# Kernel tuning notes

Hardware: AMD Instinct MI355X
Metric: run time of the kernel (lower is better)

## Reference

```python
import jax, jax.numpy as jnp
import numpy as np

E = 128      # n_routed_experts (hardcoded in DS_CONFIG_FOR_NEMOTRON)
I = 1856     # moe_intermediate_size
K = 6        # num_experts_per_tok
H = 512      # config.hidden_size
T = 4096     # flattened tokens (batch*seq)
C = 320      # per-expert capacity; avg load = T*K/E = 192, C=320 makes drops ~impossible


def setup_inputs() -> dict:
    key = jax.random.key(0)
    k1, k2, k3, k4, k5 = jax.random.split(key, 5)
    return {
        "hidden_states": jax.random.normal(k1, (T, H), jnp.float32),
        "top_k_index": jax.random.randint(k2, (T, K), 0, E, jnp.int32),
        "top_k_weights": jax.random.uniform(k3, (T, K), jnp.float32),
        "w_gate_up": jax.random.normal(k4, (E, H, 2 * I), jnp.float32) * 0.02,
        "w_down": jax.random.normal(k5, (E, I, H), jnp.float32) * 0.02,
    }


def reference(hidden_states, top_k_index, top_k_weights, w_gate_up, w_down):
    # Grouped-GEMM formulation of the naive per-expert loop: sort the (token, k)
    # pairs by expert, pack each expert's tokens into a fixed-capacity buffer,
    # run batched gate/up/down GEMMs over all experts at once, then weighted
    # scatter-add back to token order. Same math as the torch loop.
    N = T * K
    e = top_k_index.reshape(N)                      # expert id per pair
    tok = jnp.repeat(jnp.arange(T), K)              # token id per pair
    w = top_k_weights.reshape(N)

    order = jnp.argsort(e)                          # stable sort by expert
    e_s, tok_s, w_s = e[order], tok[order], w[order]

    counts = jax.ops.segment_sum(jnp.ones((N,), jnp.int32), e, num_segments=E)
    starts = jnp.cumsum(counts) - counts            # exclusive prefix sum
    pos = jnp.arange(N) - starts[e_s]               # rank within expert
    valid = pos < C                                 # capacity guard (never trips at this load)
    slot = jnp.where(valid, e_s * C + pos, E * C)   # overflow -> dummy slot

    # Dispatch: [E*C+1, H] buffer of gathered token states (dummy row absorbs overflow)
    buf = jnp.zeros((E * C + 1, H), hidden_states.dtype).at[slot].set(hidden_states[tok_s])
    x = buf[: E * C].reshape(E, C, H)

    gu = jnp.einsum('ech,ehf->ecf', x, w_gate_up)   # [E, C, 2I]
    gate, up = jnp.split(gu, 2, axis=-1)
    inter = jax.nn.silu(gate) * up                  # [E, C, I]
    y = jnp.einsum('eci,eih->ech', inter, w_down).reshape(E * C, H)

    # Combine: gather each pair's expert output, scale by router weight, scatter-add by token
    gather_idx = jnp.where(valid, e_s * C + pos, 0)
    pair_y = y[gather_idx] * jnp.where(valid, w_s, 0.0)[:, None]
    out = jnp.zeros((T, H), hidden_states.dtype).at[tok_s].add(pair_y)
    # use_context_proj=False: context states alias the hidden states
    return (out, out)
```

## Files before the change

### kernel.cpp

```cpp
#include <hip/hip_runtime.h>
#include <hip/hip_bf16.h>
#include <stdint.h>

#define NE 128
#define NI 1856
#define NKK 6
#define NH 512
#define NT 4096
#define CAP 320
#define NPAIR (NT*NKK)
#define LD2I (2*NI)

typedef unsigned short u16;
typedef __attribute__((ext_vector_type(4))) float f32x4;
typedef __attribute__((ext_vector_type(8))) short bf16x8;
typedef __attribute__((ext_vector_type(4))) short s16x4;
typedef const void __attribute__((address_space(1)))* gas1p;
typedef void __attribute__((address_space(3)))* gas3p;

__device__ __forceinline__ short f2bf(float f) {
  union { __hip_bfloat16 h; short s; } c; c.h = __float2bfloat16(f); return c.s;
}
__device__ __forceinline__ float bf2f(short s) {
  union { float f; unsigned u; } v; v.u = ((unsigned)(u16)s) << 16; return v.f;
}

__global__ void k_route(const int* __restrict__ topk, int* __restrict__ counts,
                        int* __restrict__ slot_of_pair, int* __restrict__ pair_of_slot) {
  int n = blockIdx.x * 256 + threadIdx.x;
  if (n >= NPAIR) return;
  int e = topk[n];
  int p = atomicAdd(&counts[e], 1);
  int s = (p < CAP) ? e * CAP + p : -1;
  slot_of_pair[n] = s;
  if (s >= 0) pair_of_slot[s] = n;
}

__global__ void k_gather(const float* __restrict__ hid, const int* __restrict__ counts,
                         const int* __restrict__ pair_of_slot, u16* __restrict__ xbuf) {
  int t = threadIdx.x;
  int row = blockIdx.x * 2 + (t >> 7);
  int c = t & 127;
  int e = row / CAP, p = row % CAP;
  if (p >= counts[e]) return;
  int n = pair_of_slot[row];
  int tok = n / NKK;
  f32x4 v = *(const f32x4*)(hid + (size_t)tok * NH + c * 4);
  s16x4 o;
  o[0] = f2bf(v[0]); o[1] = f2bf(v[1]); o[2] = f2bf(v[2]); o[3] = f2bf(v[3]);
  *(s16x4*)(xbuf + (size_t)row * NH + c * 4) = o;
}

__global__ __launch_bounds__(256, 2) void k_gemm1(
    const u16* __restrict__ xbuf, const float* __restrict__ wgu,
    const int* __restrict__ counts, u16* __restrict__ inter, int e0)
{
  __shared__ __align__(16) char lds[32768];
  int bid = blockIdx.x;
  int mt = bid % 3;
  int nt = (bid / 3) % 29;
  int el = bid / 87;
  int e = e0 + el;
  int cnt = counts[e];
  int row0 = mt * 128;
  if (row0 >= cnt) return;
  int n0 = nt * 64;
  int t = threadIdx.x, w = t >> 6, l = t & 63;
  int wm = w >> 1, wc = w & 1;
  const char* abase = (const char*)(xbuf + (size_t)e * CAP * NH);

  auto stage = [&](int buf, int kt) {
    char* dstb = lds + buf * 16384;
    #pragma unroll
    for (int i = 0; i < 4; ++i) {
      int seg = i * 4 + w;
      int o = seg * 1024 + l * 16;
      int r = o >> 7;
      int inner = o & 127;
      int si = inner ^ ((r & 7) << 4);
      int grow = row0 + r; grow = grow < CAP ? grow : CAP - 1;
      const char* g = abase + (size_t)grow * (NH * 2) + kt * 128 + si;
      __builtin_amdgcn_global_load_lds((gas1p)g, (gas3p)(dstb + seg * 1024), 16, 0, 0);
    }
  };

  f32x4 acc[4][4];
  #pragma unroll
  for (int m = 0; m < 4; ++m)
    #pragma unroll
    for (int b = 0; b < 4; ++b) acc[m][b] = (f32x4){0.f, 0.f, 0.f, 0.f};

  stage(0, 0);
  const float* wbase = wgu + (size_t)e * NH * LD2I + n0 + wc * 32 + (l & 15);

  for (int kt = 0; kt < 8; ++kt) {
    __syncthreads();
    if (kt + 1 < 8) stage((kt + 1) & 1, kt + 1);
    const char* abuf = lds + (kt & 1) * 16384;
    #pragma unroll
    for (int ks = 0; ks < 2; ++ks) {
      int krow = kt * 64 + ks * 32 + ((l >> 4) << 3);
      const float* bp = wbase + (size_t)krow * LD2I;
      float bv[4][8];
      #pragma unroll
      for (int nf = 0; nf < 2; ++nf)
        #pragma unroll
        for (int j = 0; j < 8; ++j) {
          bv[nf][j]     = bp[(size_t)j * LD2I + nf * 16];
          bv[2 + nf][j] = bp[(size_t)j * LD2I + nf * 16 + NI];
        }
      bf16x8 bfrag[4];
      #pragma unroll
      for (int b = 0; b < 4; ++b)
        #pragma unroll
        for (int j = 0; j < 8; ++j) bfrag[b][j] = f2bf(bv[b][j]);
      bf16x8 afrag[4];
      #pragma unroll
      for (int mf = 0; mf < 4; ++mf) {
        int r = wm * 64 + mf * 16 + (l & 15);
        int inner = (ks * 64 + ((l >> 4) << 4)) ^ ((r & 7) << 4);
        afrag[mf] = *(const bf16x8*)(abuf + r * 128 + inner);
      }
      #pragma unroll
      for (int mf = 0; mf < 4; ++mf)
        #pragma unroll
        for (int b = 0; b < 4; ++b)
          acc[mf][b] = __builtin_amdgcn_mfma_f32_16x16x32_bf16(afrag[mf], bfrag[b], acc[mf][b], 0, 0, 0);
    }
  }

  __syncthreads();

  int vmax = cnt < CAP ? cnt : CAP;
  int rmax = vmax - row0; if (rmax > 128) rmax = 128;
  char* rb = lds;
  #pragma unroll
  for (int mf = 0; mf < 4; ++mf)
    #pragma unroll
    for (int nf = 0; nf < 2; ++nf) {
      f32x4 g = acc[mf][nf], u = acc[mf][2 + nf];
      #pragma unroll
      for (int r = 0; r < 4; ++r) {
        float gv = g[r];
        float sv = gv / (1.f + __expf(-gv));
        float val = sv * u[r];
        int rl = wm * 64 + mf * 16 + ((l >> 4) << 2) + r;
        int cl = wc * 32 + nf * 16 + (l & 15);
        *(short*)(rb + rl * 128 + ((cl * 2) ^ ((rl & 7) << 4))) = f2bf(val);
      }
    }
  __syncthreads();
  u16* obase = inter + (size_t)(el * CAP + row0) * NI + n0;
  #pragma unroll
  for (int i = 0; i < 4; ++i) {
    int task = i * 256 + t;
    int r = task >> 3, part = task & 7;
    if (r < rmax) {
      bf16x8 v = *(const bf16x8*)(rb + r * 128 + ((part * 16) ^ ((r & 7) << 4)));
      *(bf16x8*)(obase + (size_t)r * NI + part * 8) = v;
    }
  }
}

__global__ __launch_bounds__(256, 2) void k_gemm2(
    const u16* __restrict__ inter, const float* __restrict__ wdn,
    const int* __restrict__ counts, u16* __restrict__ Y, int e0)
{
  __shared__ __align__(16) char lds[32768];
  int bid = blockIdx.x;
  int mt = bid % 3;
  int nt = (bid / 3) & 7;
  int el = bid / 24;
  int e = e0 + el;
  int cnt = counts[e];
  int row0 = mt * 128;
  if (row0 >= cnt) return;
  int n0 = nt * 64;
  int t = threadIdx.x, w = t >> 6, l = t & 63;
  int wm = w >> 1, wc = w & 1;
  const char* abase = (const char*)(inter + (size_t)el * CAP * NI);

  auto stage = [&](int buf, int kt) {
    char* dstb = lds + buf * 16384;
    #pragma unroll
    for (int i = 0; i < 4; ++i) {
      int seg = i * 4 + w;
      int o = seg * 1024 + l * 16;
      int r = o >> 7;
      int inner = o & 127;
      int si = inner ^ ((r & 7) << 4);
      int grow = row0 + r; grow = grow < CAP ? grow : CAP - 1;
      const char* g = abase + (size_t)grow * (NI * 2) + kt * 128 + si;
      __builtin_amdgcn_global_load_lds((gas1p)g, (gas3p)(dstb + seg * 1024), 16, 0, 0);
    }
  };

  f32x4 acc[4][2];
  #pragma unroll
  for (int m = 0; m < 4; ++m) { acc[m][0] = (f32x4){0.f,0.f,0.f,0.f}; acc[m][1] = (f32x4){0.f,0.f,0.f,0.f}; }

  stage(0, 0);
  const float* wbase = wdn + (size_t)e * NI * NH + n0 + wc * 32 + (l & 15);

  for (int kt = 0; kt < 29; ++kt) {
    __syncthreads();
    if (kt + 1 < 29) stage((kt + 1) & 1, kt + 1);
    const char* abuf = lds + (kt & 1) * 16384;
    #pragma unroll
    for (int ks = 0; ks < 2; ++ks) {
      int krow = kt * 64 + ks * 32 + ((l >> 4) << 3);
      const float* bp = wbase + (size_t)krow * NH;
      float bv[2][8];
      #pragma unroll
      for (int nf = 0; nf < 2; ++nf)
        #pragma unroll
        for (int j = 0; j < 8; ++j) bv[nf][j] = bp[(size_t)j * NH + nf * 16];
      bf16x8 bfrag[2];
      #pragma unroll
      for (int b = 0; b < 2; ++b)
        #pragma unroll
        for (int j = 0; j < 8; ++j) bfrag[b][j] = f2bf(bv[b][j]);
      bf16x8 afrag[4];
      #pragma unroll
      for (int mf = 0; mf < 4; ++mf) {
        int r = wm * 64 + mf * 16 + (l & 15);
        int inner = (ks * 64 + ((l >> 4) << 4)) ^ ((r & 7) << 4);
        afrag[mf] = *(const bf16x8*)(abuf + r * 128 + inner);
      }
      #pragma unroll
      for (int mf = 0; mf < 4; ++mf)
        #pragma unroll
        for (int b = 0; b < 2; ++b)
          acc[mf][b] = __builtin_amdgcn_mfma_f32_16x16x32_bf16(afrag[mf], bfrag[b], acc[mf][b], 0, 0, 0);
    }
  }

  __syncthreads();

  int vmax = cnt < CAP ? cnt : CAP;
  int rmax = vmax - row0; if (rmax > 128) rmax = 128;
  char* rb = lds;
  #pragma unroll
  for (int mf = 0; mf < 4; ++mf)
    #pragma unroll
    for (int nf = 0; nf < 2; ++nf) {
      f32x4 a = acc[mf][nf];
      #pragma unroll
      for (int r = 0; r < 4; ++r) {
        int rl = wm * 64 + mf * 16 + ((l >> 4) << 2) + r;
        int cl = wc * 32 + nf * 16 + (l & 15);
        *(short*)(rb + rl * 128 + ((cl * 2) ^ ((rl & 7) << 4))) = f2bf(a[r]);
      }
    }
  __syncthreads();
  u16* obase = Y + (size_t)(e * CAP + row0) * NH + n0;
  #pragma unroll
  for (int i = 0; i < 4; ++i) {
    int task = i * 256 + t;
    int r = task >> 3, part = task & 7;
    if (r < rmax) {
      bf16x8 v = *(const bf16x8*)(rb + r * 128 + ((part * 16) ^ ((r & 7) << 4)));
      *(bf16x8*)(obase + (size_t)r * NH + part * 8) = v;
    }
  }
}

__global__ void k_combine(const int* __restrict__ slot_of_pair, const float* __restrict__ wts,
                          const u16* __restrict__ Y, float* __restrict__ out)
{
  int t = threadIdx.x;
  int tok = blockIdx.x * 2 + (t >> 7);
  int c = t & 127;
  f32x4 a = (f32x4){0.f, 0.f, 0.f, 0.f};
  #pragma unroll
  for (int k = 0; k < NKK; ++k) {
    int n = tok * NKK + k;
    int s = slot_of_pair[n];
    if (s >= 0) {
      float wv = wts[n];
      s16x4 y = *(const s16x4*)(Y + (size_t)s * NH + c * 4);
      a[0] += wv * bf2f(y[0]);
      a[1] += wv * bf2f(y[1]);
      a[2] += wv * bf2f(y[2]);
      a[3] += wv * bf2f(y[3]);
    }
  }
  *(f32x4*)(out + (size_t)tok * NH + c * 4) = a;
  *(f32x4*)(out + (size_t)(NT + tok) * NH + c * 4) = a;
}

extern "C" void kernel_launch(void* const* d_in, const int* in_sizes, int n_in,
                              void* d_out, int out_size, void* d_ws, size_t ws_size,
                              hipStream_t stream) {
  const float* hid  = (const float*)d_in[0];
  const int*   topk = (const int*)d_in[1];
  const float* wts  = (const float*)d_in[2];
  const float* wgu  = (const float*)d_in[3];
  const float* wdn  = (const float*)d_in[4];

  char* ws = (char*)d_ws;
  size_t off = 0;
  auto alloc = [&](size_t sz) { char* p = ws + off; off = (off + sz + 255) & ~(size_t)255; return p; };
  int* counts        = (int*)alloc(NE * 4);
  int* slot_of_pair  = (int*)alloc((size_t)NPAIR * 4);
  int* pair_of_slot  = (int*)alloc((size_t)NE * CAP * 4);
  u16* xbuf          = (u16*)alloc((size_t)NE * CAP * NH * 2);
  u16* Y             = (u16*)alloc((size_t)NE * CAP * NH * 2);
  size_t remain = ws_size > off ? ws_size - off : 0;
  size_t per_e = (size_t)CAP * NI * 2;
  int chunkE = (int)(remain / per_e);
  if (chunkE > NE) chunkE = NE;
  if (chunkE < 1) chunkE = 1;
  u16* inter = (u16*)(ws + off);

  hipMemsetAsync(counts, 0, NE * 4, stream);
  k_route<<<NPAIR / 256, 256, 0, stream>>>(topk, counts, slot_of_pair, pair_of_slot);
  k_gather<<<NE * CAP / 2, 256, 0, stream>>>(hid, counts, pair_of_slot, xbuf);
  for (int e0 = 0; e0 < NE; e0 += chunkE) {
    int ce = NE - e0 < chunkE ? NE - e0 : chunkE;
    k_gemm1<<<ce * 29 * 3, 256, 0, stream>>>(xbuf, wgu, counts, inter, e0);
    k_gemm2<<<ce * 8 * 3, 256, 0, stream>>>(inter, wdn, counts, Y, e0);
  }
  k_combine<<<NT / 2, 256, 0, stream>>>(slot_of_pair, wts, Y, (float*)d_out);
}
```

Before: 650.9 us.

## Use 256-row M tiles with 512-thread blocks and XCD-aware block remapping

Both grouped GEMMs now use 512-thread blocks covering 256 token rows (two M tiles per expert instead of three), with 64KB LDS double buffers. This halves how often each block re-reads and re-converts the fp32 weight slice, and the weights are the dominant traffic. A block-id remap groups logical neighbours (same expert) onto the same XCD to improve L2 reuse of weights. In exchange, occupancy drops to one block per CU, and experts with fewer rows waste more of the larger tile.

```diff
diff --git a/kernel.cpp b/kernel.cpp
--- a/kernel.cpp
+++ b/kernel.cpp
@@ -23,6 +23,12 @@
 }
 __device__ __forceinline__ float bf2f(short s) {
   union { float f; unsigned u; } v; v.u = ((unsigned)(u16)s) << 16; return v.f;
+}
+
+__device__ __forceinline__ int xcd_logical(int bid, int n) {
+  int q = n >> 3, r = n & 7;
+  int xcd = bid & 7, j = bid >> 3;
+  return xcd * q + (xcd < r ? xcd : r) + j;
 }
 
 __global__ void k_route(const int* __restrict__ topk, int* __restrict__ counts,
@@ -51,18 +57,19 @@
   *(s16x4*)(xbuf + (size_t)row * NH + c * 4) = o;
 }
 
-__global__ __launch_bounds__(256, 2) void k_gemm1(
+__global__ __launch_bounds__(512, 1) void k_gemm1(
     const u16* __restrict__ xbuf, const float* __restrict__ wgu,
-    const int* __restrict__ counts, u16* __restrict__ inter, int e0)
+    const int* __restrict__ counts, u16* __restrict__ inter, int e0, int nblk)
 {
-  __shared__ __align__(16) char lds[32768];
-  int bid = blockIdx.x;
-  int mt = bid % 3;
-  int nt = (bid / 3) % 29;
-  int el = bid / 87;
+  __shared__ __align__(16) char lds[65536];
+  int L = xcd_logical(blockIdx.x, nblk);
+  int el = L / 58;
+  int inner = L % 58;
+  int nt = inner >> 1;
+  int mt = inner & 1;
   int e = e0 + el;
   int cnt = counts[e];
-  int row0 = mt * 128;
+  int row0 = mt * 256;
   if (row0 >= cnt) return;
   int n0 = nt * 64;
   int t = threadIdx.x, w = t >> 6, l = t & 63;
@@ -70,14 +77,14 @@
   const char* abase = (const char*)(xbuf + (size_t)e * CAP * NH);
 
   auto stage = [&](int buf, int kt) {
-    char* dstb = lds + buf * 16384;
+    char* dstb = lds + buf * 32768;
     #pragma unroll
     for (int i = 0; i < 4; ++i) {
-      int seg = i * 4 + w;
+      int seg = i * 8 + w;
       int o = seg * 1024 + l * 16;
       int r = o >> 7;
-      int inner = o & 127;
-      int si = inner ^ ((r & 7) << 4);
+      int inr = o & 127;
+      int si = inr ^ ((r & 7) << 4);
       int grow = row0 + r; grow = grow < CAP ? grow : CAP - 1;
       const char* g = abase + (size_t)grow * (NH * 2) + kt * 128 + si;
       __builtin_amdgcn_global_load_lds((gas1p)g, (gas3p)(dstb + seg * 1024), 16, 0, 0);
@@ -96,7 +103,7 @@
   for (int kt = 0; kt < 8; ++kt) {
     __syncthreads();
     if (kt + 1 < 8) stage((kt + 1) & 1, kt + 1);
-    const char* abuf = lds + (kt & 1) * 16384;
+    const char* abuf = lds + (kt & 1) * 32768;
     #pragma unroll
     for (int ks = 0; ks < 2; ++ks) {
       int krow = kt * 64 + ks * 32 + ((l >> 4) << 3);
@@ -118,8 +125,8 @@
       #pragma unroll
       for (int mf = 0; mf < 4; ++mf) {
         int r = wm * 64 + mf * 16 + (l & 15);
-        int inner = (ks * 64 + ((l >> 4) << 4)) ^ ((r & 7) << 4);
-        afrag[mf] = *(const bf16x8*)(abuf + r * 128 + inner);
+        int inr = (ks * 64 + ((l >> 4) << 4)) ^ ((r & 7) << 4);
+        afrag[mf] = *(const bf16x8*)(abuf + r * 128 + inr);
       }
       #pragma unroll
       for (int mf = 0; mf < 4; ++mf)
@@ -132,7 +139,7 @@
   __syncthreads();
 
   int vmax = cnt < CAP ? cnt : CAP;
-  int rmax = vmax - row0; if (rmax > 128) rmax = 128;
+  int rmax = vmax - row0; if (rmax > 256) rmax = 256;
   char* rb = lds;
   #pragma unroll
   for (int mf = 0; mf < 4; ++mf)
@@ -153,7 +160,7 @@
   u16* obase = inter + (size_t)(el * CAP + row0) * NI + n0;
   #pragma unroll
   for (int i = 0; i < 4; ++i) {
-    int task = i * 256 + t;
+    int task = i * 512 + t;
     int r = task >> 3, part = task & 7;
     if (r < rmax) {
       bf16x8 v = *(const bf16x8*)(rb + r * 128 + ((part * 16) ^ ((r & 7) << 4)));
@@ -162,18 +169,19 @@
   }
 }
 
-__global__ __launch_bounds__(256, 2) void k_gemm2(
+__global__ __launch_bounds__(512, 1) void k_gemm2(
     const u16* __restrict__ inter, const float* __restrict__ wdn,
-    const int* __restrict__ counts, u16* __restrict__ Y, int e0)
+    const int* __restrict__ counts, u16* __restrict__ Y, int e0, int nblk)
 {
-  __shared__ __align__(16) char lds[32768];
-  int bid = blockIdx.x;
-  int mt = bid % 3;
-  int nt = (bid / 3) & 7;
-  int el = bid / 24;
+  __shared__ __align__(16) char lds[65536];
+  int L = xcd_logical(blockIdx.x, nblk);
+  int el = L / 16;
+  int inner = L % 16;
+  int nt = inner >> 1;
+  int mt = inner & 1;
   int e = e0 + el;
   int cnt = counts[e];
-  int row0 = mt * 128;
+  int row0 = mt * 256;
   if (row0 >= cnt) return;
   int n0 = nt * 64;
   int t = threadIdx.x, w = t >> 6, l = t & 63;
@@ -181,14 +189,14 @@
   const char* abase = (const char*)(inter + (size_t)el * CAP * NI);
 
   auto stage = [&](int buf, int kt) {
-    char* dstb = lds + buf * 16384;
+    char* dstb = lds + buf * 32768;
     #pragma unroll
     for (int i = 0; i < 4; ++i) {
-      int seg = i * 4 + w;
+      int seg = i * 8 + w;
       int o = seg * 1024 + l * 16;
       int r = o >> 7;
-      int inner = o & 127;
-      int si = inner ^ ((r & 7) << 4);
+      int inr = o & 127;
+      int si = inr ^ ((r & 7) << 4);
       int grow = row0 + r; grow = grow < CAP ? grow : CAP - 1;
       const char* g = abase + (size_t)grow * (NI * 2) + kt * 128 + si;
       __builtin_amdgcn_global_load_lds((gas1p)g, (gas3p)(dstb + seg * 1024), 16, 0, 0);
@@ -205,7 +213,7 @@
   for (int kt = 0; kt < 29; ++kt) {
     __syncthreads();
     if (kt + 1 < 29) stage((kt + 1) & 1, kt + 1);
-    const char* abuf = lds + (kt & 1) * 16384;
+    const char* abuf = lds + (kt & 1) * 32768;
     #pragma unroll
     for (int ks = 0; ks < 2; ++ks) {
       int krow = kt * 64 + ks * 32 + ((l >> 4) << 3);
@@ -224,8 +232,8 @@
       #pragma unroll
       for (int mf = 0; mf < 4; ++mf) {
         int r = wm * 64 + mf * 16 + (l & 15);
-        int inner = (ks * 64 + ((l >> 4) << 4)) ^ ((r & 7) << 4);
-        afrag[mf] = *(const bf16x8*)(abuf + r * 128 + inner);
+        int inr = (ks * 64 + ((l >> 4) << 4)) ^ ((r & 7) << 4);
+        afrag[mf] = *(const bf16x8*)(abuf + r * 128 + inr);
       }
       #pragma unroll
       for (int mf = 0; mf < 4; ++mf)
@@ -238,7 +246,7 @@
   __syncthreads();
 
   int vmax = cnt < CAP ? cnt : CAP;
-  int rmax = vmax - row0; if (rmax > 128) rmax = 128;
+  int rmax = vmax - row0; if (rmax > 256) rmax = 256;
   char* rb = lds;
   #pragma unroll
   for (int mf = 0; mf < 4; ++mf)
@@ -256,7 +264,7 @@
   u16* obase = Y + (size_t)(e * CAP + row0) * NH + n0;
   #pragma unroll
   for (int i = 0; i < 4; ++i) {
-    int task = i * 256 + t;
+    int task = i * 512 + t;
     int r = task >> 3, part = task & 7;
     if (r < rmax) {
       bf16x8 v = *(const bf16x8*)(rb + r * 128 + ((part * 16) ^ ((r & 7) << 4)));
@@ -318,8 +326,10 @@
   k_gather<<<NE * CAP / 2, 256, 0, stream>>>(hid, counts, pair_of_slot, xbuf);
   for (int e0 = 0; e0 < NE; e0 += chunkE) {
     int ce = NE - e0 < chunkE ? NE - e0 : chunkE;
-    k_gemm1<<<ce * 29 * 3, 256, 0, stream>>>(xbuf, wgu, counts, inter, e0);
-    k_gemm2<<<ce * 8 * 3, 256, 0, stream>>>(inter, wdn, counts, Y, e0);
+    int nb1 = ce * 58;
+    int nb2 = ce * 16;
+    k_gemm1<<<nb1, 512, 0, stream>>>(xbuf, wgu, counts, inter, e0, nb1);
+    k_gemm2<<<nb2, 512, 0, stream>>>(inter, wdn, counts, Y, e0, nb2);
   }
   k_combine<<<NT / 2, 256, 0, stream>>>(slot_of_pair, wts, Y, (float*)d_out);
 }
```

New measurement: 1.067 ms. 1.64x slower.

## Restructure expert GEMMs: 256-row M tiles, LDS-staged B, XCD-aware block mapping

Applied to the files above, without the earlier changes.

Both expert GEMM kernels now cover all of an expert's rows (up to 256 per pass, looping when more) inside one block. The fp32 weight tile is converted to bf16 once and staged in LDS, so it is no longer reloaded by three separate M-tile blocks and each wave no longer converts its own B fragments. Block indices are remapped so that consecutive logical tiles land on the same XCD, which improves L2 locality for the weights. The changes also shrink the K step to 32, double-buffer B in LDS, and raise occupancy to 3 blocks per CU. The cost is more LDS per block and fewer blocks per launch, and rows 256-320 need a second, mostly empty pass.

```diff
diff --git a/kernel.cpp b/kernel.cpp
--- a/kernel.cpp
+++ b/kernel.cpp
@@ -23,6 +23,12 @@
 }
 __device__ __forceinline__ float bf2f(short s) {
   union { float f; unsigned u; } v; v.u = ((unsigned)(u16)s) << 16; return v.f;
+}
+
+__device__ __forceinline__ int xcd_logical(int bid, int n) {
+  int q = n >> 3, r = n & 7;
+  int xcd = bid & 7, j = bid >> 3;
+  return xcd * q + (xcd < r ? xcd : r) + j;
 }
 
 __global__ void k_route(const int* __restrict__ topk, int* __restrict__ counts,
@@ -51,216 +57,225 @@
   *(s16x4*)(xbuf + (size_t)row * NH + c * 4) = o;
 }
 
-__global__ __launch_bounds__(256, 2) void k_gemm1(
+__global__ __launch_bounds__(256, 3) void k_gemm1(
     const u16* __restrict__ xbuf, const float* __restrict__ wgu,
-    const int* __restrict__ counts, u16* __restrict__ inter, int e0)
+    const int* __restrict__ counts, u16* __restrict__ inter, int e0, int nblk)
 {
-  __shared__ __align__(16) char lds[32768];
-  int bid = blockIdx.x;
-  int mt = bid % 3;
-  int nt = (bid / 3) % 29;
-  int el = bid / 87;
+  __shared__ __align__(16) char lds[40960];
+  int L = xcd_logical(blockIdx.x, nblk);
+  int el = L / 58, nt = L % 58;
   int e = e0 + el;
-  int cnt = counts[e];
-  int row0 = mt * 128;
-  if (row0 >= cnt) return;
-  int n0 = nt * 64;
+  int cnt = counts[e]; if (cnt > CAP) cnt = CAP;
+  int n0 = nt * 32;
   int t = threadIdx.x, w = t >> 6, l = t & 63;
   int wm = w >> 1, wc = w & 1;
   const char* abase = (const char*)(xbuf + (size_t)e * CAP * NH);
 
-  auto stage = [&](int buf, int kt) {
-    char* dstb = lds + buf * 16384;
+  int bc = t & 63, bkc = t >> 6;
+  int gcol = (bc < 32) ? (n0 + bc) : (NI + n0 + (bc - 32));
+  const float* bsrc = wgu + (size_t)e * NH * LD2I + gcol;
+  float bv[8];
+
+  int kg16 = (l >> 4) * 16;
+  int bcol0 = wc * 16 + (l & 15);
+  int bswz = ((bcol0 & 3) << 4);
+
+  for (int base = 0; base < cnt; base += 256) {
+    __syncthreads();
+
+    auto stageA = [&](int buf, int kt) {
+      char* dstb = lds + buf * 16384;
+      #pragma unroll
+      for (int i = 0; i < 4; ++i) {
+        int seg = i * 4 + w;
+        int o = seg * 1024 + l * 16;
+        int r = o >> 6, slot = o & 63;
+        int grow = base + r; if (grow > CAP - 1) grow = CAP - 1;
+        const char* g = abase + (size_t)grow * (NH * 2) + kt * 64 + (slot ^ ((r & 3) << 4));
+        __builtin_amdgcn_global_load_lds((gas1p)g, (gas3p)(dstb + seg * 1024), 16, 0, 0);
+      }
+    };
+    auto loadB = [&](int kt) {
+      const float* p = bsrc + (size_t)(kt * 32 + bkc * 8) * LD2I;
+      #pragma unroll
+      for (int j = 0; j < 8; ++j) bv[j] = p[(size_t)j * LD2I];
+    };
+    auto writeB = [&](int buf) {
+      bf16x8 o;
+      #pragma unroll
+      for (int j = 0; j < 8; ++j) o[j] = f2bf(bv[j]);
+      char* bb = lds + 32768 + buf * 4096;
+      *(bf16x8*)(bb + bc * 64 + ((bkc * 16) ^ ((bc & 3) << 4))) = o;
+    };
+
+    f32x4 acc[2][4][2];
+    #pragma unroll
+    for (int m = 0; m < 2; ++m)
+      #pragma unroll
+      for (int f = 0; f < 4; ++f) { acc[m][f][0] = (f32x4){0,0,0,0}; acc[m][f][1] = (f32x4){0,0,0,0}; }
+
+    loadB(0);
+    stageA(0, 0);
+    writeB(0);
+
+    for (int kt = 0; kt < 16; ++kt) {
+      __syncthreads();
+      int cur = kt & 1, nxt = cur ^ 1;
+      if (kt + 1 < 16) { loadB(kt + 1); stageA(nxt, kt + 1); }
+      const char* ab = lds + cur * 16384;
+      const char* bb = lds + 32768 + cur * 4096;
+      bf16x8 bg = *(const bf16x8*)(bb + bcol0 * 64 + (kg16 ^ bswz));
+      bf16x8 bu = *(const bf16x8*)(bb + (32 + bcol0) * 64 + (kg16 ^ bswz));
+      #pragma unroll
+      for (int mt = 0; mt < 2; ++mt)
+        #pragma unroll
+        for (int mf = 0; mf < 4; ++mf) {
+          int r = mt * 128 + wm * 64 + mf * 16 + (l & 15);
+          bf16x8 af = *(const bf16x8*)(ab + r * 64 + (kg16 ^ ((r & 3) << 4)));
+          acc[mt][mf][0] = __builtin_amdgcn_mfma_f32_16x16x32_bf16(af, bg, acc[mt][mf][0], 0, 0, 0);
+          acc[mt][mf][1] = __builtin_amdgcn_mfma_f32_16x16x32_bf16(af, bu, acc[mt][mf][1], 0, 0, 0);
+        }
+      if (kt + 1 < 16) writeB(nxt);
+    }
+
+    __syncthreads();
+
+    int cl = wc * 16 + (l & 15);
+    #pragma unroll
+    for (int mt = 0; mt < 2; ++mt)
+      #pragma unroll
+      for (int mf = 0; mf < 4; ++mf) {
+        f32x4 g = acc[mt][mf][0], u = acc[mt][mf][1];
+        #pragma unroll
+        for (int r = 0; r < 4; ++r) {
+          float gv = g[r];
+          float val = gv / (1.f + __expf(-gv)) * u[r];
+          int rl = mt * 128 + wm * 64 + mf * 16 + (l >> 4) * 4 + r;
+          *(short*)(lds + rl * 64 + ((cl * 2) ^ ((rl & 3) << 4))) = f2bf(val);
+        }
+      }
+    __syncthreads();
+    int rmax = cnt - base; if (rmax > 256) rmax = 256;
+    u16* obase = inter + (size_t)(el * CAP + base) * NI + n0;
     #pragma unroll
     for (int i = 0; i < 4; ++i) {
-      int seg = i * 4 + w;
-      int o = seg * 1024 + l * 16;
-      int r = o >> 7;
-      int inner = o & 127;
-      int si = inner ^ ((r & 7) << 4);
-      int grow = row0 + r; grow = grow < CAP ? grow : CAP - 1;
-      const char* g = abase + (size_t)grow * (NH * 2) + kt * 128 + si;
-      __builtin_amdgcn_global_load_lds((gas1p)g, (gas3p)(dstb + seg * 1024), 16, 0, 0);
-    }
-  };
-
-  f32x4 acc[4][4];
-  #pragma unroll
-  for (int m = 0; m < 4; ++m)
-    #pragma unroll
-    for (int b = 0; b < 4; ++b) acc[m][b] = (f32x4){0.f, 0.f, 0.f, 0.f};
-
-  stage(0, 0);
-  const float* wbase = wgu + (size_t)e * NH * LD2I + n0 + wc * 32 + (l & 15);
-
-  for (int kt = 0; kt < 8; ++kt) {
-    __syncthreads();
-    if (kt + 1 < 8) stage((kt + 1) & 1, kt + 1);
-    const char* abuf = lds + (kt & 1) * 16384;
-    #pragma unroll
-    for (int ks = 0; ks < 2; ++ks) {
-      int krow = kt * 64 + ks * 32 + ((l >> 4) << 3);
-      const float* bp = wbase + (size_t)krow * LD2I;
-      float bv[4][8];
-      #pragma unroll
-      for (int nf = 0; nf < 2; ++nf)
-        #pragma unroll
-        for (int j = 0; j < 8; ++j) {
-          bv[nf][j]     = bp[(size_t)j * LD2I + nf * 16];
-          bv[2 + nf][j] = bp[(size_t)j * LD2I + nf * 16 + NI];
-        }
-      bf16x8 bfrag[4];
-      #pragma unroll
-      for (int b = 0; b < 4; ++b)
-        #pragma unroll
-        for (int j = 0; j < 8; ++j) bfrag[b][j] = f2bf(bv[b][j]);
-      bf16x8 afrag[4];
-      #pragma unroll
-      for (int mf = 0; mf < 4; ++mf) {
-        int r = wm * 64 + mf * 16 + (l & 15);
-        int inner = (ks * 64 + ((l >> 4) << 4)) ^ ((r & 7) << 4);
-        afrag[mf] = *(const bf16x8*)(abuf + r * 128 + inner);
-      }
-      #pragma unroll
-      for (int mf = 0; mf < 4; ++mf)
-        #pragma unroll
-        for (int b = 0; b < 4; ++b)
-          acc[mf][b] = __builtin_amdgcn_mfma_f32_16x16x32_bf16(afrag[mf], bfrag[b], acc[mf][b], 0, 0, 0);
+      int task = i * 256 + t;
+      int r = task >> 2, p = task & 3;
+      if (r < rmax) {
+        bf16x8 v = *(const bf16x8*)(lds + r * 64 + ((p * 16) ^ ((r & 3) << 4)));
+        *(bf16x8*)(obase + (size_t)r * NI + p * 8) = v;
+      }
     }
   }
-
-  __syncthreads();
-
-  int vmax = cnt < CAP ? cnt : CAP;
-  int rmax = vmax - row0; if (rmax > 128) rmax = 128;
-  char* rb = lds;
-  #pragma unroll
-  for (int mf = 0; mf < 4; ++mf)
-    #pragma unroll
-    for (int nf = 0; nf < 2; ++nf) {
-      f32x4 g = acc[mf][nf], u = acc[mf][2 + nf];
-      #pragma unroll
-      for (int r = 0; r < 4; ++r) {
-        float gv = g[r];
-        float sv = gv / (1.f + __expf(-gv));
-        float val = sv * u[r];
-        int rl = wm * 64 + mf * 16 + ((l >> 4) << 2) + r;
-        int cl = wc * 32 + nf * 16 + (l & 15);
-        *(short*)(rb + rl * 128 + ((cl * 2) ^ ((rl & 7) << 4))) = f2bf(val);
-      }
-    }
-  __syncthreads();
-  u16* obase = inter + (size_t)(el * CAP + row0) * NI + n0;
-  #pragma unroll
-  for (int i = 0; i < 4; ++i) {
-    int task = i * 256 + t;
-    int r = task >> 3, part = task & 7;
-    if (r < rmax) {
-      bf16x8 v = *(const bf16x8*)(rb + r * 128 + ((part * 16) ^ ((r & 7) << 4)));
-      *(bf16x8*)(obase + (size_t)r * NI + part * 8) = v;
-    }
-  }
-}
-
-__global__ __launch_bounds__(256, 2) void k_gemm2(
+}
+
+__global__ __launch_bounds__(256, 3) void k_gemm2(
     const u16* __restrict__ inter, const float* __restrict__ wdn,
-    const int* __restrict__ counts, u16* __restrict__ Y, int e0)
+    const int* __restrict__ counts, u16* __restrict__ Y, int e0, int nblk)
 {
-  __shared__ __align__(16) char lds[32768];
-  int bid = blockIdx.x;
-  int mt = bid % 3;
-  int nt = (bid / 3) & 7;
-  int el = bid / 24;
+  __shared__ __align__(16) char lds[40960];
+  int L = xcd_logical(blockIdx.x, nblk);
+  int el = L / 8, nt = L % 8;
   int e = e0 + el;
-  int cnt = counts[e];
-  int row0 = mt * 128;
-  if (row0 >= cnt) return;
+  int cnt = counts[e]; if (cnt > CAP) cnt = CAP;
   int n0 = nt * 64;
   int t = threadIdx.x, w = t >> 6, l = t & 63;
   int wm = w >> 1, wc = w & 1;
   const char* abase = (const char*)(inter + (size_t)el * CAP * NI);
 
-  auto stage = [&](int buf, int kt) {
-    char* dstb = lds + buf * 16384;
-    #pragma unroll
-    for (int i = 0; i < 4; ++i) {
-      int seg = i * 4 + w;
-      int o = seg * 1024 + l * 16;
-      int r = o >> 7;
-      int inner = o & 127;
-      int si = inner ^ ((r & 7) << 4);
-      int grow = row0 + r; grow = grow < CAP ? grow : CAP - 1;
-      const char* g = abase + (size_t)grow * (NI * 2) + kt * 128 + si;
-      __builtin_amdgcn_global_load_lds((gas1p)g, (gas3p)(dstb + seg * 1024), 16, 0, 0);
-    }
-  };
-
-  f32x4 acc[4][2];
-  #pragma unroll
-  for (int m = 0; m < 4; ++m) { acc[m][0] = (f32x4){0.f,0.f,0.f,0.f}; acc[m][1] = (f32x4){0.f,0.f,0.f,0.f}; }
-
-  stage(0, 0);
-  const float* wbase = wdn + (size_t)e * NI * NH + n0 + wc * 32 + (l & 15);
-
-  for (int kt = 0; kt < 29; ++kt) {
-    __syncthreads();
-    if (kt + 1 < 29) stage((kt + 1) & 1, kt + 1);
-    const char* abuf = lds + (kt & 1) * 16384;
-    #pragma unroll
-    for (int ks = 0; ks < 2; ++ks) {
-      int krow = kt * 64 + ks * 32 + ((l >> 4) << 3);
-      const float* bp = wbase + (size_t)krow * NH;
-      float bv[2][8];
-      #pragma unroll
-      for (int nf = 0; nf < 2; ++nf)
+  int bc = t & 63, bkc = t >> 6;
+  const float* bsrc = wdn + (size_t)e * NI * NH + n0 + bc;
+  float bv[8];
+
+  int kg16 = (l >> 4) * 16;
+  int bcol0 = wc * 32 + (l & 15);
+  int bswz = ((bcol0 & 3) << 4);
+
+  for (int base = 0; base < cnt; base += 256) {
+    __syncthreads();
+
+    auto stageA = [&](int buf, int kt) {
+      char* dstb = lds + buf * 16384;
+      #pragma unroll
+      for (int i = 0; i < 4; ++i) {
+        int seg = i * 4 + w;
+        int o = seg * 1024 + l * 16;
+        int r = o >> 6, slot = o & 63;
+        int grow = base + r; if (grow > CAP - 1) grow = CAP - 1;
+        const char* g = abase + (size_t)grow * (NI * 2) + kt * 64 + (slot ^ ((r & 3) << 4));
+        __builtin_amdgcn_global_load_lds((gas1p)g, (gas3p)(dstb + seg * 1024), 16, 0, 0);
+      }
+    };
+    auto loadB = [&](int kt) {
+      const float* p = bsrc + (size_t)(kt * 32 + bkc * 8) * NH;
+      #pragma unroll
+      for (int j = 0; j < 8; ++j) bv[j] = p[(size_t)j * NH];
+    };
+    auto writeB = [&](int buf) {
+      bf16x8 o;
+      #pragma unroll
+      for (int j = 0; j < 8; ++j) o[j] = f2bf(bv[j]);
+      char* bb = lds + 32768 + buf * 4096;
+      *(bf16x8*)(bb + bc * 64 + ((bkc * 16) ^ ((bc & 3) << 4))) = o;
+    };
+
+    f32x4 acc[2][4][2];
+    #pragma unroll
+    for (int m = 0; m < 2; ++m)
+      #pragma unroll
+      for (int f = 0; f < 4; ++f) { acc[m][f][0] = (f32x4){0,0,0,0}; acc[m][f][1] = (f32x4){0,0,0,0}; }
+
+    loadB(0);
+    stageA(0, 0);
+    writeB(0);
+
+    for (int kt = 0; kt < 58; ++kt) {
+      __syncthreads();
+      int cur = kt & 1, nxt = cur ^ 1;
+      if (kt + 1 < 58) { loadB(kt + 1); stageA(nxt, kt + 1); }
+      const char* ab = lds + cur * 16384;
+      const char* bb = lds + 32768 + cur * 4096;
+      bf16x8 b0 = *(const bf16x8*)(bb + bcol0 * 64 + (kg16 ^ bswz));
+      bf16x8 b1 = *(const bf16x8*)(bb + (16 + bcol0) * 64 + (kg16 ^ bswz));
+      #pragma unroll
+      for (int mt = 0; mt < 2; ++mt)
         #pragma unroll
-        for (int j = 0; j < 8; ++j) bv[nf][j] = bp[(size_t)j * NH + nf * 16];
-      bf16x8 bfrag[2];
-      #pragma unroll
-      for (int b = 0; b < 2; ++b)
-        #pragma unroll
-        for (int j = 0; j < 8; ++j) bfrag[b][j] = f2bf(bv[b][j]);
-      bf16x8 afrag[4];
-      #pragma unroll
-      for (int mf = 0; mf < 4; ++mf) {
-        int r = wm * 64 + mf * 16 + (l & 15);
-        int inner = (ks * 64 + ((l >> 4) << 4)) ^ ((r & 7) << 4);
-        afrag[mf] = *(const bf16x8*)(abuf + r * 128 + inner);
-      }
+        for (int mf = 0; mf < 4; ++mf) {
+          int r = mt * 128 + wm * 64 + mf * 16 + (l & 15);
+          bf16x8 af = *(const bf16x8*)(ab + r * 64 + (kg16 ^ ((r & 3) << 4)));
+          acc[mt][mf][0] = __builtin_amdgcn_mfma_f32_16x16x32_bf16(af, b0, acc[mt][mf][0], 0, 0, 0);
+          acc[mt][mf][1] = __builtin_amdgcn_mfma_f32_16x16x32_bf16(af, b1, acc[mt][mf][1], 0, 0, 0);
+        }
+      if (kt + 1 < 58) writeB(nxt);
+    }
+
+    __syncthreads();
+
+    #pragma unroll
+    for (int mt = 0; mt < 2; ++mt)
       #pragma unroll
       for (int mf = 0; mf < 4; ++mf)
         #pragma unroll
-        for (int b = 0; b < 2; ++b)
-          acc[mf][b] = __builtin_amdgcn_mfma_f32_16x16x32_bf16(afrag[mf], bfrag[b], acc[mf][b], 0, 0, 0);
-    }
-  }
-
-  __syncthreads();
-
-  int vmax = cnt < CAP ? cnt : CAP;
-  int rmax = vmax - row0; if (rmax > 128) rmax = 128;
-  char* rb = lds;
-  #pragma unroll
-  for (int mf = 0; mf < 4; ++mf)
-    #pragma unroll
-    for (int nf = 0; nf < 2; ++nf) {
-      f32x4 a = acc[mf][nf];
-      #pragma unroll
-      for (int r = 0; r < 4; ++r) {
-        int rl = wm * 64 + mf * 16 + ((l >> 4) << 2) + r;
-        int cl = wc * 32 + nf * 16 + (l & 15);
-        *(short*)(rb + rl * 128 + ((cl * 2) ^ ((rl & 7) << 4))) = f2bf(a[r]);
-      }
-    }
-  __syncthreads();
-  u16* obase = Y + (size_t)(e * CAP + row0) * NH + n0;
-  #pragma unroll
-  for (int i = 0; i < 4; ++i) {
-    int task = i * 256 + t;
-    int r = task >> 3, part = task & 7;
-    if (r < rmax) {
-      bf16x8 v = *(const bf16x8*)(rb + r * 128 + ((part * 16) ^ ((r & 7) << 4)));
-      *(bf16x8*)(obase + (size_t)r * NH + part * 8) = v;
+        for (int f = 0; f < 2; ++f) {
+          f32x4 a = acc[mt][mf][f];
+          int cl = wc * 32 + f * 16 + (l & 15);
+          #pragma unroll
+          for (int r = 0; r < 4; ++r) {
+            int rl = mt * 128 + wm * 64 + mf * 16 + (l >> 4) * 4 + r;
+            *(short*)(lds + rl * 128 + ((cl * 2) ^ ((rl & 7) << 4))) = f2bf(a[r]);
+          }
+        }
+    __syncthreads();
+    int rmax = cnt - base; if (rmax > 256) rmax = 256;
+    u16* obase = Y + (size_t)(e * CAP + base) * NH + n0;
+    #pragma unroll
+    for (int i = 0; i < 8; ++i) {
+      int task = i * 256 + t;
+      int r = task >> 3, p = task & 7;
+      if (r < rmax) {
+        bf16x8 v = *(const bf16x8*)(lds + r * 128 + ((p * 16) ^ ((r & 7) << 4)));
+        *(bf16x8*)(obase + (size_t)r * NH + p * 8) = v;
+      }
     }
   }
 }
@@ -318,8 +333,10 @@
   k_gather<<<NE * CAP / 2, 256, 0, stream>>>(hid, counts, pair_of_slot, xbuf);
   for (int e0 = 0; e0 < NE; e0 += chunkE) {
     int ce = NE - e0 < chunkE ? NE - e0 : chunkE;
-    k_gemm1<<<ce * 29 * 3, 256, 0, stream>>>(xbuf, wgu, counts, inter, e0);
-    k_gemm2<<<ce * 8 * 3, 256, 0, stream>>>(inter, wdn, counts, Y, e0);
+    int nb1 = ce * 58;
+    int nb2 = ce * 8;
+    k_gemm1<<<nb1, 256, 0, stream>>>(xbuf, wgu, counts, inter, e0, nb1);
+    k_gemm2<<<nb2, 256, 0, stream>>>(inter, wdn, counts, Y, e0, nb2);
   }
   k_combine<<<NT / 2, 256, 0, stream>>>(slot_of_pair, wts, Y, (float*)d_out);
 }
```

After: 642.5 us. About the same (-1.3%).
